# Optimization experiments

Measured on AMD Instinct MI355X. Metric: run time of the kernel, lower is better.

## Reference

```python
import jax, jax.numpy as jnp
import numpy as np

D_MODEL = 1024
N_HEADS = 16
D_K = D_MODEL // N_HEADS


def setup_inputs() -> dict:
    key = jax.random.key(0)
    ks = jax.random.split(key, 11)
    B, S = 2, 2048
    scale = 1.0 / np.sqrt(D_MODEL)
    return {
        "query": jax.random.normal(ks[0], (B, S, D_MODEL), jnp.float32),
        "key": jax.random.normal(ks[1], (B, S, D_MODEL), jnp.float32),
        "value": jax.random.normal(ks[2], (B, S, D_MODEL), jnp.float32),
        "w_q": jax.random.normal(ks[3], (D_MODEL, D_MODEL), jnp.float32) * scale,
        "b_q": jnp.zeros((D_MODEL,), jnp.float32),
        "w_k": jax.random.normal(ks[4], (D_MODEL, D_MODEL), jnp.float32) * scale,
        "b_k": jnp.zeros((D_MODEL,), jnp.float32),
        "w_v": jax.random.normal(ks[5], (D_MODEL, D_MODEL), jnp.float32) * scale,
        "b_v": jnp.zeros((D_MODEL,), jnp.float32),
        "w_o": jax.random.normal(ks[6], (D_MODEL, D_MODEL), jnp.float32) * scale,
        "b_o": jnp.zeros((D_MODEL,), jnp.float32),
    }


def reference(query, key, value, w_q, b_q, w_k, b_k, w_v, b_v, w_o, b_o):
    B, S, _ = query.shape
    # Linear projections (torch Linear: x @ W.T + b), split heads -> (B, H, S, Dk)
    def proj(x, w, b):
        y = jnp.einsum('bsd,ed->bse', x, w) + b
        return y.reshape(B, -1, N_HEADS, D_K).transpose(0, 2, 1, 3)
    q = proj(query, w_q, b_q)
    k = proj(key, w_k, b_k)
    v = proj(value, w_v, b_v)
    # Scaled dot-product attention (full O(S^2) scores, faithful to source)
    scores = jnp.einsum('bhqd,bhkd->bhqk', q, k) / np.sqrt(D_K)
    attn = jax.nn.softmax(scores, axis=-1)
    out = jnp.einsum('bhqk,bhkd->bhqd', attn, v)  # (B, H, S, Dk)
    out = out.transpose(0, 2, 1, 3).reshape(B, S, D_MODEL)
    out = jnp.einsum('bsd,ed->bse', out, w_o) + b_o
    return out
```

## Files before the change

### kernel.cpp

```cpp
#include <hip/hip_runtime.h>
#include <hip/hip_bf16.h>

#define DM 1024
#define NH 16
#define DKH 64
#define BB 2
#define SS 2048
#define MM (BB*SS)
#define HKB 1024

typedef __bf16 v8bf __attribute__((ext_vector_type(8)));
typedef float  v4f  __attribute__((ext_vector_type(4)));
typedef float  v16f __attribute__((ext_vector_type(16)));

__device__ __forceinline__ unsigned short f2bf(float f) {
    union { float f; unsigned int u; } v; v.f = f;
    unsigned int u = v.u;
    unsigned int r = (u + 0x7fffu + ((u >> 16) & 1u)) >> 16;
    return (unsigned short)r;
}

__device__ __forceinline__ int cvtpk(float lo, float hi) {
    int r;
    asm("v_cvt_pk_bf16_f32 %0, %1, %2" : "=v"(r) : "v"(lo), "v"(hi));
    return r;
}

__device__ __forceinline__ void pl32swap(int& a, int& b) {
    asm("v_permlane32_swap_b32 %0, %1" : "+v"(a), "+v"(b));
}

__device__ __forceinline__ void gl16(const unsigned short* g, unsigned short* l) {
    auto gp = reinterpret_cast<const __attribute__((address_space(1))) unsigned int*>(
        reinterpret_cast<uintptr_t>(g));
    auto lp = reinterpret_cast<__attribute__((address_space(3))) unsigned int*>(
        reinterpret_cast<uintptr_t>(l));
    __builtin_amdgcn_global_load_lds(gp, lp, 16, 0, 0);
}

__global__ __launch_bounds__(256) void cvt_w(
    const float* __restrict__ wq, const float* __restrict__ wk, const float* __restrict__ wv,
    const float* __restrict__ wo, unsigned short* __restrict__ dst)
{
    const int y = blockIdx.y;
    const float* src = (y == 0) ? wq : (y == 1) ? wk : (y == 2) ? wv : wo;
    unsigned short* d = dst + (size_t)y * DM * DM;
    const size_t n = (size_t)DM * DM;
    const size_t stride = (size_t)gridDim.x * blockDim.x;
    for (size_t i = (size_t)blockIdx.x * blockDim.x + threadIdx.x; i * 8 < n; i += stride) {
        float4 a = ((const float4*)src)[2 * i];
        float4 b = ((const float4*)src)[2 * i + 1];
        uint4 o;
        o.x = (unsigned)cvtpk(a.x, a.y);
        o.y = (unsigned)cvtpk(a.z, a.w);
        o.z = (unsigned)cvtpk(b.x, b.y);
        o.w = (unsigned)cvtpk(b.z, b.w);
        ((uint4*)d)[i] = o;
    }
}

__global__ __launch_bounds__(256) void proj_qkv_b(
    const float* __restrict__ Xq, const float* __restrict__ Xk, const float* __restrict__ Xv,
    const unsigned short* __restrict__ wb,
    const float* __restrict__ bq, const float* __restrict__ bk, const float* __restrict__ bv,
    unsigned short* __restrict__ q_ws, unsigned short* __restrict__ k_ws,
    unsigned short* __restrict__ vt_ws)
{
    const int z = blockIdx.z;
    const float* X = (z == 0) ? Xq : (z == 1) ? Xk : Xv;
    const unsigned short* W = wb + (size_t)z * DM * DM;
    const float* bias = (z == 0) ? bq : (z == 1) ? bk : bv;

    __shared__ unsigned short lA[2][128 * 32];
    __shared__ unsigned short lB[3][128 * 32];

    const int t = threadIdx.x;
    const int lane = t & 63, w = t >> 6;
    const int wm = w >> 1, wn = w & 1;
    const int g = lane >> 4, lr = lane & 15;

    const int hid = blockIdx.y * 8 + blockIdx.x;
    const int xcd = hid & 7, slot = hid >> 3;
    const int mbase = (xcd * 4 + (slot & 3)) * 128;
    const int nbase = (slot >> 2) * 128;

    const int srow = lane >> 2;
    const int scol = (lane & 3) * 8;
    const int arow = t >> 1;
    const int acg  = (t & 1) * 16;

    v4f acc[4][4];
#pragma unroll
    for (int i = 0; i < 4; ++i)
#pragma unroll
        for (int j = 0; j < 4; ++j)
            acc[i][j] = (v4f){0.f, 0.f, 0.f, 0.f};

    float4 ar0, ar1, ar2, ar3;
    auto loadA = [&](int kb) {
        const float4* p = (const float4*)(X + (size_t)(mbase + arow) * DM + kb + acg);
        ar0 = p[0]; ar1 = p[1]; ar2 = p[2]; ar3 = p[3];
    };
    auto writeA = [&](int bi) {
        uint4 o0, o1;
        o0.x = (unsigned)cvtpk(ar0.x, ar0.y); o0.y = (unsigned)cvtpk(ar0.z, ar0.w);
        o0.z = (unsigned)cvtpk(ar1.x, ar1.y); o0.w = (unsigned)cvtpk(ar1.z, ar1.w);
        o1.x = (unsigned)cvtpk(ar2.x, ar2.y); o1.y = (unsigned)cvtpk(ar2.z, ar2.w);
        o1.z = (unsigned)cvtpk(ar3.x, ar3.y); o1.w = (unsigned)cvtpk(ar3.z, ar3.w);
        *(uint4*)&lA[bi][arow * 32 + acg]     = o0;
        *(uint4*)&lA[bi][arow * 32 + acg + 8] = o1;
    };
    auto stageB = [&](int bi, int kb) {
        gl16(W + (size_t)(nbase + w * 16 + srow) * DM + kb + scol,      &lB[bi][w * 512]);
        gl16(W + (size_t)(nbase + 64 + w * 16 + srow) * DM + kb + scol, &lB[bi][(w + 4) * 512]);
    };
    auto compute = [&](const unsigned short* A_, const unsigned short* B_) {
        v8bf af[4], bf4[4];
#pragma unroll
        for (int mt = 0; mt < 4; ++mt)
            af[mt] = *(const v8bf*)(&A_[(wm * 64 + mt * 16 + lr) * 32 + g * 8]);
#pragma unroll
        for (int nt = 0; nt < 4; ++nt)
            bf4[nt] = *(const v8bf*)(&B_[(wn * 64 + nt * 16 + lr) * 32 + g * 8]);
#pragma unroll
        for (int mt = 0; mt < 4; ++mt)
#pragma unroll
            for (int nt = 0; nt < 4; ++nt)
                acc[mt][nt] = __builtin_amdgcn_mfma_f32_16x16x32_bf16(af[mt], bf4[nt], acc[mt][nt], 0, 0, 0);
    };

    loadA(0);
    stageB(0, 0);
    writeA(0);
    loadA(32);
    stageB(1, 32);

#pragma unroll 1
    for (int ki = 0; ki < 31; ++ki) {
        writeA((ki + 1) & 1);
        if (ki < 30) {
            loadA((ki + 2) * 32);
            stageB((ki + 2) % 3, (ki + 2) * 32);
            asm volatile("s_waitcnt vmcnt(6) lgkmcnt(0)" ::: "memory");
        } else {
            asm volatile("s_waitcnt vmcnt(0) lgkmcnt(0)" ::: "memory");
        }
        __builtin_amdgcn_sched_barrier(0);
        __builtin_amdgcn_s_barrier();
        __builtin_amdgcn_sched_barrier(0);
        compute(lA[ki & 1], lB[ki % 3]);
        __builtin_amdgcn_sched_barrier(0);
        __builtin_amdgcn_s_barrier();
    }
    compute(lA[31 & 1], lB[31 % 3]);

    const float scale = (z == 0) ? 0.18033688011112042f : 1.0f;
#pragma unroll
    for (int nt = 0; nt < 4; ++nt) {
        int e = nbase + wn * 64 + nt * 16 + lr;
        float bval = bias[e];
        int h = e >> 6, dk = e & 63;
#pragma unroll
        for (int mt = 0; mt < 4; ++mt) {
#pragma unroll
            for (int r = 0; r < 4; ++r) {
                int m = mbase + wm * 64 + mt * 16 + g * 4 + r;
                float val = (acc[mt][nt][r] + bval) * scale;
                unsigned short o = f2bf(val);
                int b = m >> 11, s = m & 2047;
                if (z == 2) {
                    vt_ws[((size_t)(b * NH + h) * DKH + dk) * SS + s] = o;
                } else {
                    unsigned short* dst = (z == 0) ? q_ws : k_ws;
                    dst[((size_t)(b * NH + h) * SS + s) * DKH + dk] = o;
                }
            }
        }
    }
}

#define KB 64
#define LDP 72
#define TILE 4608

__global__ __launch_bounds__(512, 4) void attn_kernel(
    const unsigned short* __restrict__ q_ws, const unsigned short* __restrict__ k_ws,
    const unsigned short* __restrict__ vt_ws, unsigned short* __restrict__ o_ws)
{
    __shared__ __align__(16) unsigned short lsBuf[2 * 4 * TILE];

    const int t = threadIdx.x, l = t & 63, w = t >> 6;
    const int h = l >> 5, ql = l & 31;
    const int qg = w >> 1, hf = w & 1;

    const int hid = blockIdx.x;
    const int slot = hid >> 3;
    const int bh = (hid & 7) * 4 + (slot & 3);
    const int qp = slot >> 2;
    const int q0 = qp * 128 + qg * 32;

    const unsigned short* Kb = k_ws + (size_t)bh * SS * DKH;
    const unsigned short* Vb = vt_ws + (size_t)bh * DKH * SS;

    v8bf qf[4];
#pragma unroll
    for (int c = 0; c < 4; ++c)
        qf[c] = *(const v8bf*)(q_ws + ((size_t)bh * SS + q0 + ql) * DKH + c * 16 + h * 8);

    v16f oT[2];
#pragma unroll
    for (int d = 0; d < 2; ++d)
#pragma unroll
        for (int r = 0; r < 16; ++r) oT[d][r] = 0.f;
    float l_lane = 0.f;
    const v16f z16 = {};

    const int r0s = t >> 3, c0s = (t & 7) * 8;
    uint4 k0r, k1r, v0r, v1r;

    k0r = *(const uint4*)(Kb + (size_t)(r0s) * DKH + c0s);
    v0r = *(const uint4*)(Vb + (size_t)r0s * SS + c0s);
    k1r = *(const uint4*)(Kb + (size_t)(HKB + r0s) * DKH + c0s);
    v1r = *(const uint4*)(Vb + (size_t)r0s * SS + HKB + c0s);
    {
        unsigned short* B0 = lsBuf;
        *(uint4*)&B0[0 * TILE + r0s * LDP + c0s] = k0r;
        *(uint4*)&B0[1 * TILE + r0s * LDP + c0s] = v0r;
        *(uint4*)&B0[2 * TILE + r0s * LDP + c0s] = k1r;
        *(uint4*)&B0[3 * TILE + r0s * LDP + c0s] = v1r;
    }
    k0r = *(const uint4*)(Kb + (size_t)(KB + r0s) * DKH + c0s);
    v0r = *(const uint4*)(Vb + (size_t)r0s * SS + KB + c0s);
    k1r = *(const uint4*)(Kb + (size_t)(HKB + KB + r0s) * DKH + c0s);
    v1r = *(const uint4*)(Vb + (size_t)r0s * SS + HKB + KB + c0s);
    asm volatile("s_waitcnt lgkmcnt(0)" ::: "memory");
    __builtin_amdgcn_sched_barrier(0);
    __builtin_amdgcn_s_barrier();
    __builtin_amdgcn_sched_barrier(0);

    const int NT = 16;
    int p = 0;
    for (int tt = 0; tt < NT; ++tt) {
        unsigned short* Kp = lsBuf + p * (4 * TILE) + hf * (2 * TILE);
        unsigned short* Vp = Kp + TILE;
        if (tt + 1 < NT) {
            unsigned short* Bn = lsBuf + (p ^ 1) * (4 * TILE);
            *(uint4*)&Bn[0 * TILE + r0s * LDP + c0s] = k0r;
            *(uint4*)&Bn[1 * TILE + r0s * LDP + c0s] = v0r;
            *(uint4*)&Bn[2 * TILE + r0s * LDP + c0s] = k1r;
            *(uint4*)&Bn[3 * TILE + r0s * LDP + c0s] = v1r;
        }
        if (tt + 2 < NT) {
            int kt2 = (tt + 2) * KB;
            k0r = *(const uint4*)(Kb + (size_t)(kt2 + r0s) * DKH + c0s);
            v0r = *(const uint4*)(Vb + (size_t)r0s * SS + kt2 + c0s);
            k1r = *(const uint4*)(Kb + (size_t)(HKB + kt2 + r0s) * DKH + c0s);
            v1r = *(const uint4*)(Vb + (size_t)r0s * SS + HKB + kt2 + c0s);
        }

        v16f sT[2];
        __builtin_amdgcn_s_setprio(1);
#pragma unroll
        for (int kb = 0; kb < 2; ++kb) {
            v8bf kf = *(const v8bf*)&Kp[(kb * 32 + ql) * LDP + h * 8];
            sT[kb] = __builtin_amdgcn_mfma_f32_32x32x16_bf16(kf, qf[0], z16, 0, 0, 0);
        }
#pragma unroll
        for (int c = 1; c < 4; ++c)
#pragma unroll
            for (int kb = 0; kb < 2; ++kb) {
                v8bf kf = *(const v8bf*)&Kp[(kb * 32 + ql) * LDP + c * 16 + h * 8];
                sT[kb] = __builtin_amdgcn_mfma_f32_32x32x16_bf16(kf, qf[c], sT[kb], 0, 0, 0);
            }
        __builtin_amdgcn_s_setprio(0);

        v8bf pfrag[4];
#pragma unroll
        for (int kb = 0; kb < 2; ++kb) {
            float rs0 = 0.f, rs1 = 0.f, rs2 = 0.f, rs3 = 0.f;
#pragma unroll
            for (int r = 0; r < 16; r += 4) {
                float e0 = __builtin_amdgcn_exp2f(sT[kb][r + 0]);
                float e1 = __builtin_amdgcn_exp2f(sT[kb][r + 1]);
                float e2 = __builtin_amdgcn_exp2f(sT[kb][r + 2]);
                float e3 = __builtin_amdgcn_exp2f(sT[kb][r + 3]);
                sT[kb][r + 0] = e0; sT[kb][r + 1] = e1;
                sT[kb][r + 2] = e2; sT[kb][r + 3] = e3;
                rs0 += e0; rs1 += e1; rs2 += e2; rs3 += e3;
            }
            l_lane += (rs0 + rs1) + (rs2 + rs3);

#pragma unroll
            for (int cc = 0; cc < 2; ++cc) {
                int A0 = cvtpk(sT[kb][8 * cc + 0], sT[kb][8 * cc + 1]);
                int A1 = cvtpk(sT[kb][8 * cc + 2], sT[kb][8 * cc + 3]);
                int B0 = cvtpk(sT[kb][8 * cc + 4], sT[kb][8 * cc + 5]);
                int B1 = cvtpk(sT[kb][8 * cc + 6], sT[kb][8 * cc + 7]);
                pl32swap(A0, B0);
                pl32swap(A1, B1);
                union { int i[4]; v8bf v; } u;
                u.i[0] = A0; u.i[1] = A1; u.i[2] = B0; u.i[3] = B1;
                pfrag[kb * 2 + cc] = u.v;
            }

            __builtin_amdgcn_s_setprio(1);
#pragma unroll
            for (int db = 0; db < 2; ++db)
#pragma unroll
                for (int cc = 0; cc < 2; ++cc) {
                    int c = kb * 2 + cc;
                    v8bf vf = *(const v8bf*)&Vp[(db * 32 + ql) * LDP + c * 16 + h * 8];
                    oT[db] = __builtin_amdgcn_mfma_f32_32x32x16_bf16(vf, pfrag[c], oT[db], 0, 0, 0);
                }
            __builtin_amdgcn_s_setprio(0);
        }

        asm volatile("s_waitcnt lgkmcnt(0)" ::: "memory");
        __builtin_amdgcn_sched_barrier(0);
        __builtin_amdgcn_s_barrier();
        __builtin_amdgcn_sched_barrier(0);
        p ^= 1;
    }

    float lsum = l_lane + __shfl_xor(l_lane, 32);
    float* lsf = (float*)lsBuf;
    const int row = qg * 32 + ql;
#pragma unroll
    for (int db = 0; db < 2; ++db)
#pragma unroll
        for (int r = 0; r < 16; ++r) {
            int d = db * 32 + (r & 3) + 8 * (r >> 2) + 4 * h;
            lsf[(hf * 128 + row) * 65 + d] = oT[db][r];
        }
    if (h == 0) lsf[(hf * 128 + row) * 65 + 64] = lsum;
    __syncthreads();

    const int orow = t >> 2;
    const int ck = t & 3;
    const float* e0 = lsf + orow * 65;
    const float* e1 = lsf + (128 + orow) * 65;
    const float linv = 1.0f / (e0[64] + e1[64]);
    const int b = bh >> 4, hh = bh & 15;
    const int d0 = ck * 16;
    unsigned short* op = o_ws + ((size_t)b * SS + qp * 128 + orow) * DM + hh * DKH + d0;
    uint4 o0, o1;
    o0.x = (unsigned)cvtpk((e0[d0+0]+e1[d0+0])*linv,  (e0[d0+1]+e1[d0+1])*linv);
    o0.y = (unsigned)cvtpk((e0[d0+2]+e1[d0+2])*linv,  (e0[d0+3]+e1[d0+3])*linv);
    o0.z = (unsigned)cvtpk((e0[d0+4]+e1[d0+4])*linv,  (e0[d0+5]+e1[d0+5])*linv);
    o0.w = (unsigned)cvtpk((e0[d0+6]+e1[d0+6])*linv,  (e0[d0+7]+e1[d0+7])*linv);
    o1.x = (unsigned)cvtpk((e0[d0+8]+e1[d0+8])*linv,  (e0[d0+9]+e1[d0+9])*linv);
    o1.y = (unsigned)cvtpk((e0[d0+10]+e1[d0+10])*linv,(e0[d0+11]+e1[d0+11])*linv);
    o1.z = (unsigned)cvtpk((e0[d0+12]+e1[d0+12])*linv,(e0[d0+13]+e1[d0+13])*linv);
    o1.w = (unsigned)cvtpk((e0[d0+14]+e1[d0+14])*linv,(e0[d0+15]+e1[d0+15])*linv);
    *(uint4*)op = o0;
    *(uint4*)(op + 8) = o1;
}

__global__ __launch_bounds__(256) void proj_o_b(
    const unsigned short* __restrict__ A, const unsigned short* __restrict__ W,
    const float* __restrict__ bo, float* __restrict__ out)
{
    __shared__ unsigned short lA[3][128 * 32];
    __shared__ unsigned short lB[3][64 * 32];

    const int t = threadIdx.x;
    const int lane = t & 63, w = t >> 6;
    const int wm = w >> 1, wn = w & 1;
    const int g = lane >> 4, lr = lane & 15;

    const int hid = blockIdx.y * 16 + blockIdx.x;
    const int xcd = hid & 7, slot = hid >> 3;
    const int mbase = (xcd * 4 + (slot & 3)) * 128;
    const int nbase = (slot >> 2) * 64;

    const int srow = lane >> 2;
    const int scol = (lane & 3) * 8;

    v4f acc[4][2];
#pragma unroll
    for (int i = 0; i < 4; ++i)
#pragma unroll
        for (int j = 0; j < 2; ++j)
            acc[i][j] = (v4f){0.f, 0.f, 0.f, 0.f};

    auto stage = [&](int bi, int kb) {
        gl16(A + (size_t)(mbase + w * 16 + srow) * DM + kb + scol,      &lA[bi][w * 512]);
        gl16(A + (size_t)(mbase + 64 + w * 16 + srow) * DM + kb + scol, &lA[bi][(w + 4) * 512]);
        gl16(W + (size_t)(nbase + w * 16 + srow) * DM + kb + scol,      &lB[bi][w * 512]);
    };
    auto compute = [&](int bi) {
        v8bf af[4], bf4[2];
#pragma unroll
        for (int mt = 0; mt < 4; ++mt)
            af[mt] = *(const v8bf*)(&lA[bi][(wm * 64 + mt * 16 + lr) * 32 + g * 8]);
#pragma unroll
        for (int nt = 0; nt < 2; ++nt)
            bf4[nt] = *(const v8bf*)(&lB[bi][(wn * 32 + nt * 16 + lr) * 32 + g * 8]);
#pragma unroll
        for (int mt = 0; mt < 4; ++mt)
#pragma unroll
            for (int nt = 0; nt < 2; ++nt)
                acc[mt][nt] = __builtin_amdgcn_mfma_f32_16x16x32_bf16(af[mt], bf4[nt], acc[mt][nt], 0, 0, 0);
    };

    stage(0, 0);
    stage(1, 32);
    int bcur = 0;
#pragma unroll 1
    for (int ki = 0; ki < 30; ++ki) {
        int bnext = bcur + 2; if (bnext >= 3) bnext -= 3;
        stage(bnext, (ki + 2) * 32);
        asm volatile("s_waitcnt vmcnt(6)" ::: "memory");
        __builtin_amdgcn_sched_barrier(0);
        __builtin_amdgcn_s_barrier();
        __builtin_amdgcn_sched_barrier(0);
        compute(bcur);
        __builtin_amdgcn_sched_barrier(0);
        __builtin_amdgcn_s_barrier();
        bcur = (bcur == 2) ? 0 : bcur + 1;
    }
    asm volatile("s_waitcnt vmcnt(3)" ::: "memory");
    __builtin_amdgcn_sched_barrier(0);
    __builtin_amdgcn_s_barrier();
    __builtin_amdgcn_sched_barrier(0);
    compute(bcur);
    __builtin_amdgcn_sched_barrier(0);
    __builtin_amdgcn_s_barrier();
    bcur = (bcur == 2) ? 0 : bcur + 1;
    asm volatile("s_waitcnt vmcnt(0)" ::: "memory");
    __builtin_amdgcn_sched_barrier(0);
    __builtin_amdgcn_s_barrier();
    __builtin_amdgcn_sched_barrier(0);
    compute(bcur);

#pragma unroll
    for (int nt = 0; nt < 2; ++nt) {
        int e = nbase + wn * 32 + nt * 16 + lr;
        float bval = bo[e];
#pragma unroll
        for (int mt = 0; mt < 4; ++mt) {
#pragma unroll
            for (int r = 0; r < 4; ++r) {
                int m = mbase + wm * 64 + mt * 16 + g * 4 + r;
                out[(size_t)m * DM + e] = acc[mt][nt][r] + bval;
            }
        }
    }
}

extern "C" void kernel_launch(void* const* d_in, const int* in_sizes, int n_in,
                              void* d_out, int out_size, void* d_ws, size_t ws_size,
                              hipStream_t stream) {
    const float* q  = (const float*)d_in[0];
    const float* k  = (const float*)d_in[1];
    const float* v  = (const float*)d_in[2];
    const float* wq = (const float*)d_in[3];
    const float* bq = (const float*)d_in[4];
    const float* wk = (const float*)d_in[5];
    const float* bk = (const float*)d_in[6];
    const float* wv = (const float*)d_in[7];
    const float* bv = (const float*)d_in[8];
    const float* wo = (const float*)d_in[9];
    const float* bo = (const float*)d_in[10];
    float* out = (float*)d_out;

    unsigned short* ws    = (unsigned short*)d_ws;
    unsigned short* q_ws  = ws;
    unsigned short* k_ws  = q_ws + (size_t)MM * DM;
    unsigned short* vt_ws = k_ws + (size_t)MM * DM;
    unsigned short* wb    = vt_ws + (size_t)MM * DM;
    unsigned short* o_ws  = wb + (size_t)4 * DM * DM;

    cvt_w<<<dim3(64, 4), 256, 0, stream>>>(wq, wk, wv, wo, wb);
    proj_qkv_b<<<dim3(8, 32, 3), 256, 0, stream>>>(q, k, v, wb, bq, bk, bv, q_ws, k_ws, vt_ws);
    attn_kernel<<<dim3(512), 512, 0, stream>>>(q_ws, k_ws, vt_ws, o_ws);
    proj_o_b<<<dim3(16, 32), 256, 0, stream>>>(o_ws, wb + (size_t)3 * DM * DM, bo, out);
}
```

Before: 117.3 us.

## Stage fp32 activations via async global_load_lds with swizzle, convert at fragment load

The QKV projection kernel now stages fp32 activation tiles straight into LDS with global_load_lds (XOR-swizzled columns) in a 3-deep ring shared with the weight tiles. Previously each thread loaded them into registers, converted to bf16 and wrote LDS. Conversion to bf16 now happens when MFMA fragments are read from LDS. This removes register staging and VGPR pressure and lets the whole pipeline run asynchronously. In exchange it doubles LDS footprint and traffic for A, and each wave repeats the conversion on every fragment read.

Measured after the change: 117.4 us. No clear change (+0.1%).

```diff
diff --git a/kernel.cpp b/kernel.cpp
--- a/kernel.cpp
+++ b/kernel.cpp
@@ -30,7 +30,7 @@
     asm("v_permlane32_swap_b32 %0, %1" : "+v"(a), "+v"(b));
 }
 
-__device__ __forceinline__ void gl16(const unsigned short* g, unsigned short* l) {
+__device__ __forceinline__ void gl16(const void* g, void* l) {
     auto gp = reinterpret_cast<const __attribute__((address_space(1))) unsigned int*>(
         reinterpret_cast<uintptr_t>(g));
     auto lp = reinterpret_cast<__attribute__((address_space(3))) unsigned int*>(
@@ -71,7 +71,7 @@
     const unsigned short* W = wb + (size_t)z * DM * DM;
     const float* bias = (z == 0) ? bq : (z == 1) ? bk : bv;
 
-    __shared__ unsigned short lA[2][128 * 32];
+    __shared__ float lAf[3][128 * 32];
     __shared__ unsigned short lB[3][128 * 32];
 
     const int t = threadIdx.x;
@@ -86,8 +86,8 @@
 
     const int srow = lane >> 2;
     const int scol = (lane & 3) * 8;
-    const int arow = t >> 1;
-    const int acg  = (t & 1) * 16;
+    const int ar  = lane >> 3;
+    const int acs = (lane & 7) ^ ar;
 
     v4f acc[4][4];
 #pragma unroll
@@ -96,32 +96,33 @@
         for (int j = 0; j < 4; ++j)
             acc[i][j] = (v4f){0.f, 0.f, 0.f, 0.f};
 
-    float4 ar0, ar1, ar2, ar3;
-    auto loadA = [&](int kb) {
-        const float4* p = (const float4*)(X + (size_t)(mbase + arow) * DM + kb + acg);
-        ar0 = p[0]; ar1 = p[1]; ar2 = p[2]; ar3 = p[3];
-    };
-    auto writeA = [&](int bi) {
-        uint4 o0, o1;
-        o0.x = (unsigned)cvtpk(ar0.x, ar0.y); o0.y = (unsigned)cvtpk(ar0.z, ar0.w);
-        o0.z = (unsigned)cvtpk(ar1.x, ar1.y); o0.w = (unsigned)cvtpk(ar1.z, ar1.w);
-        o1.x = (unsigned)cvtpk(ar2.x, ar2.y); o1.y = (unsigned)cvtpk(ar2.z, ar2.w);
-        o1.z = (unsigned)cvtpk(ar3.x, ar3.y); o1.w = (unsigned)cvtpk(ar3.z, ar3.w);
-        *(uint4*)&lA[bi][arow * 32 + acg]     = o0;
-        *(uint4*)&lA[bi][arow * 32 + acg + 8] = o1;
+    auto stageA = [&](int bi, int kb) {
+#pragma unroll
+        for (int i = 0; i < 4; ++i) {
+            const float* gp = X + (size_t)(mbase + w * 32 + i * 8 + ar) * DM + kb + acs * 4;
+            gl16(gp, &lAf[bi][(w * 32 + i * 8) * 32]);
+        }
     };
     auto stageB = [&](int bi, int kb) {
         gl16(W + (size_t)(nbase + w * 16 + srow) * DM + kb + scol,      &lB[bi][w * 512]);
         gl16(W + (size_t)(nbase + 64 + w * 16 + srow) * DM + kb + scol, &lB[bi][(w + 4) * 512]);
     };
-    auto compute = [&](const unsigned short* A_, const unsigned short* B_) {
+    auto compute = [&](int bi) {
         v8bf af[4], bf4[4];
 #pragma unroll
-        for (int mt = 0; mt < 4; ++mt)
-            af[mt] = *(const v8bf*)(&A_[(wm * 64 + mt * 16 + lr) * 32 + g * 8]);
+        for (int mt = 0; mt < 4; ++mt) {
+            int r = wm * 64 + mt * 16 + lr;
+            int rs = r & 7;
+            float4 fa = *(const float4*)&lAf[bi][r * 32 + (((2 * g)     ^ rs) << 2)];
+            float4 fb = *(const float4*)&lAf[bi][r * 32 + (((2 * g + 1) ^ rs) << 2)];
+            union { int i[4]; v8bf v; } u;
+            u.i[0] = cvtpk(fa.x, fa.y); u.i[1] = cvtpk(fa.z, fa.w);
+            u.i[2] = cvtpk(fb.x, fb.y); u.i[3] = cvtpk(fb.z, fb.w);
+            af[mt] = u.v;
+        }
 #pragma unroll
         for (int nt = 0; nt < 4; ++nt)
-            bf4[nt] = *(const v8bf*)(&B_[(wn * 64 + nt * 16 + lr) * 32 + g * 8]);
+            bf4[nt] = *(const v8bf*)(&lB[bi][(wn * 64 + nt * 16 + lr) * 32 + g * 8]);
 #pragma unroll
         for (int mt = 0; mt < 4; ++mt)
 #pragma unroll
@@ -129,30 +130,36 @@
                 acc[mt][nt] = __builtin_amdgcn_mfma_f32_16x16x32_bf16(af[mt], bf4[nt], acc[mt][nt], 0, 0, 0);
     };
 
-    loadA(0);
-    stageB(0, 0);
-    writeA(0);
-    loadA(32);
-    stageB(1, 32);
-
+    stageA(0, 0);   stageB(0, 0);
+    stageA(1, 32);  stageB(1, 32);
+    int bcur = 0;
 #pragma unroll 1
-    for (int ki = 0; ki < 31; ++ki) {
-        writeA((ki + 1) & 1);
-        if (ki < 30) {
-            loadA((ki + 2) * 32);
-            stageB((ki + 2) % 3, (ki + 2) * 32);
-            asm volatile("s_waitcnt vmcnt(6) lgkmcnt(0)" ::: "memory");
-        } else {
-            asm volatile("s_waitcnt vmcnt(0) lgkmcnt(0)" ::: "memory");
-        }
+    for (int ki = 0; ki < 30; ++ki) {
+        int bnext = bcur + 2; if (bnext >= 3) bnext -= 3;
+        stageA(bnext, (ki + 2) * 32);
+        stageB(bnext, (ki + 2) * 32);
+        asm volatile("s_waitcnt vmcnt(12)" ::: "memory");
         __builtin_amdgcn_sched_barrier(0);
         __builtin_amdgcn_s_barrier();
         __builtin_amdgcn_sched_barrier(0);
-        compute(lA[ki & 1], lB[ki % 3]);
+        compute(bcur);
         __builtin_amdgcn_sched_barrier(0);
         __builtin_amdgcn_s_barrier();
-    }
-    compute(lA[31 & 1], lB[31 % 3]);
+        bcur = (bcur == 2) ? 0 : bcur + 1;
+    }
+    asm volatile("s_waitcnt vmcnt(6)" ::: "memory");
+    __builtin_amdgcn_sched_barrier(0);
+    __builtin_amdgcn_s_barrier();
+    __builtin_amdgcn_sched_barrier(0);
+    compute(bcur);
+    __builtin_amdgcn_sched_barrier(0);
+    __builtin_amdgcn_s_barrier();
+    bcur = (bcur == 2) ? 0 : bcur + 1;
+    asm volatile("s_waitcnt vmcnt(0)" ::: "memory");
+    __builtin_amdgcn_sched_barrier(0);
+    __builtin_amdgcn_s_barrier();
+    __builtin_amdgcn_sched_barrier(0);
+    compute(bcur);
 
     const float scale = (z == 0) ? 0.18033688011112042f : 1.0f;
 #pragma unroll
```
